# Performance work log

Hardware: AMD Instinct MI355X
Metric: run time of the kernel (lower is better)

The kernel has to match this reference:

```python
import jax, jax.numpy as jnp
import numpy as np

N_NODES = 100000
N_EDGES = 1600000
IN_DIM, HID_DIM, OUT_DIM = 128, 64, 64
NEG_SLOPE = 0.2


def _gat_layer(h_in, src, dst, W, a_src, a_dst, b, n_nodes):
    # h: [N, F_out]
    h = h_in @ W.T
    alpha_src = h @ a_src  # [N]
    alpha_dst = h @ a_dst  # [N]
    # per-edge raw attention logits (edge j->i: src=j, dst=i)
    e = jax.nn.leaky_relu(alpha_src[src] + alpha_dst[dst], NEG_SLOPE)  # [E]
    # segment softmax over incoming edges of each dst node
    m = jax.ops.segment_max(e, dst, num_segments=n_nodes)
    ex = jnp.exp(e - m[dst])
    denom = jax.ops.segment_sum(ex, dst, num_segments=n_nodes)
    alpha = ex / denom[dst]  # [E], denom > 0 thanks to self-loops
    out = jax.ops.segment_sum(h[src] * alpha[:, None], dst, num_segments=n_nodes)
    return out + b


def setup_inputs() -> dict:
    key = jax.random.key(0)
    ks = jax.random.split(key, 12)
    x = jax.random.normal(ks[0], (N_NODES, IN_DIM), dtype=jnp.float32)
    edge_index = jax.random.randint(ks[1], (2, N_EDGES), 0, N_NODES)
    edge_attr = jax.random.normal(ks[2], (N_EDGES, 1), dtype=jnp.float32)
    s1 = 1.0 / np.sqrt(IN_DIM)
    s2 = 1.0 / np.sqrt(HID_DIM)
    W1 = jax.random.normal(ks[3], (HID_DIM, IN_DIM), dtype=jnp.float32) * s1
    att_src1 = jax.random.normal(ks[4], (HID_DIM,), dtype=jnp.float32) * s2
    att_dst1 = jax.random.normal(ks[5], (HID_DIM,), dtype=jnp.float32) * s2
    b1 = jnp.zeros((HID_DIM,), dtype=jnp.float32)
    W2 = jax.random.normal(ks[6], (OUT_DIM, HID_DIM), dtype=jnp.float32) * s2
    att_src2 = jax.random.normal(ks[7], (OUT_DIM,), dtype=jnp.float32) * s2
    att_dst2 = jax.random.normal(ks[8], (OUT_DIM,), dtype=jnp.float32) * s2
    b2 = jnp.zeros((OUT_DIM,), dtype=jnp.float32)
    return {"x": x, "edge_index": edge_index, "edge_attr": edge_attr,
            "W1": W1, "att_src1": att_src1, "att_dst1": att_dst1, "b1": b1,
            "W2": W2, "att_src2": att_src2, "att_dst2": att_dst2, "b2": b2}


def reference(x, edge_index, edge_attr, W1, att_src1, att_dst1, b1,
              W2, att_src2, att_dst2, b2):
    n = x.shape[0]
    # add self-loops (PyG GATConv default); edge_attr unused (edge_dim=None)
    loop = jnp.arange(n, dtype=edge_index.dtype)
    src = jnp.concatenate([edge_index[0], loop])
    dst = jnp.concatenate([edge_index[1], loop])
    h = _gat_layer(x, src, dst, W1, att_src1, att_dst1, b1, n)
    h = jax.nn.relu(h)
    h = _gat_layer(h, src, dst, W2, att_src2, att_dst2, b2, n)
    # global_mean_pool with batch=None -> mean over all nodes, shape [1, F]
    return jnp.mean(h, axis=0, keepdims=True)
```

## Files before the change

kernel.cpp:

```cpp
#include <hip/hip_runtime.h>

#define NEG_SLOPE 0.2f
#define BSHIFT 6
#define NBMAX 2048
#define BCAP 1408
#define CHUNK 8192

__device__ __forceinline__ unsigned short f2b(float x) {
    unsigned u = __float_as_uint(x);
    u += 0x7fff + ((u >> 16) & 1);
    return (unsigned short)(u >> 16);
}
__device__ __forceinline__ float b2f(unsigned short u) {
    return __uint_as_float((unsigned)u << 16);
}

__global__ __launch_bounds__(256) void bin_fixed_kernel(
    const int* __restrict__ ei, int* __restrict__ bcnt,
    int* __restrict__ binned, int E, int NB)
{
    __shared__ int cnt1[NBMAX], rsv[NBMAX], cnt2[NBMAX];
    const int tid = threadIdx.x;
    for (int i = tid; i < NB; i += 256) { cnt1[i] = 0; cnt2[i] = 0; }
    __syncthreads();
    const int start = blockIdx.x * CHUNK;
    const int end = min(start + CHUNK, E);
    for (int i = start + tid; i < end; i += 256)
        atomicAdd(&cnt1[ei[E + i] >> BSHIFT], 1);
    __syncthreads();
    for (int i = tid; i < NB; i += 256)
        rsv[i] = cnt1[i] ? atomicAdd(&bcnt[i], cnt1[i]) : 0;
    __syncthreads();
    for (int i = start + tid; i < end; i += 256) {
        int s = ei[i], d = ei[E + i];
        int b = d >> BSHIFT;
        int r = rsv[b] + atomicAdd(&cnt2[b], 1);
        if (r < BCAP) binned[(size_t)b * BCAP + r] = (s << BSHIFT) | (d & 63);
    }
}

__global__ __launch_bounds__(256) void bscan_kernel(
    const int* __restrict__ bcnt, int* __restrict__ bbase, int NB)
{
    __shared__ int lds[256];
    const int t = threadIdx.x;
    int v[8]; int s = 0;
    #pragma unroll
    for (int j = 0; j < 8; ++j) {
        int i = t * 8 + j;
        v[j] = (i < NB) ? bcnt[i] : 0;
        s += v[j];
    }
    lds[t] = s;
    __syncthreads();
    #pragma unroll
    for (int off = 1; off < 256; off <<= 1) {
        int x = (t >= off) ? lds[t - off] : 0;
        __syncthreads();
        lds[t] += x;
        __syncthreads();
    }
    int excl = (t > 0) ? lds[t - 1] : 0;
    #pragma unroll
    for (int j = 0; j < 8; ++j) {
        int i = t * 8 + j;
        if (i < NB) { bbase[i] = excl + 64 * i; excl += v[j]; }
    }
}

__global__ __launch_bounds__(256) void bucket_csr_kernel(
    const int* __restrict__ binned, const int* __restrict__ bcnt,
    const int* __restrict__ bbase, int* __restrict__ row_ptr,
    int* __restrict__ esrc, int N)
{
    __shared__ int ldeg[64];
    __shared__ int lcur[64];
    const int b = blockIdx.x;
    const int tid = threadIdx.x;
    const int node0 = b << BSHIFT;
    const int cnt = min(bcnt[b], BCAP);
    const int base_e = bbase[b];
    const int* bp = binned + (size_t)b * BCAP;

    if (tid < 64) ldeg[tid] = (node0 + tid < N) ? 1 : 0;
    __syncthreads();
    for (int i = tid; i < cnt; i += 256)
        atomicAdd(&ldeg[bp[i] & 63], 1);
    __syncthreads();
    if (tid < 64) {
        int v = ldeg[tid];
        int inc = v;
        #pragma unroll
        for (int off = 1; off < 64; off <<= 1) {
            int t2 = __shfl_up(inc, off, 64);
            if (tid >= off) inc += t2;
        }
        int excl = inc - v;
        int node = node0 + tid;
        if (node <= N) row_ptr[node] = base_e + excl;
        if (node < N) {
            esrc[base_e + excl] = node;
            lcur[tid] = base_e + excl + 1;
        }
    }
    __syncthreads();
    for (int i = tid; i < cnt; i += 256) {
        int v = bp[i];
        int pos = atomicAdd(&lcur[v & 63], 1);
        esrc[pos] = v >> BSHIFT;
    }
}

template<int K>
__global__ __launch_bounds__(256) void gemm_attn_kernel(
    const float* __restrict__ in, const float* __restrict__ W,
    const float* __restrict__ a_src, const float* __restrict__ a_dst,
    unsigned short* __restrict__ hb, float* __restrict__ asrc,
    float* __restrict__ adst, int N)
{
    constexpr int KB = 64;
    constexpr int NKC = KB / 4;
    constexpr int LDN = 65;
    __shared__ float4 xs4[NKC * LDN];
    __shared__ float4 ws4[NKC * LDN];
    __shared__ float avs[64], avd[64];

    const int tid = threadIdx.x;
    const int node0 = blockIdx.x * 64;
    const int tf = tid & 15;
    const int tn = tid >> 4;

    if (tid < 64) { avs[tid] = a_src[tid]; avd[tid] = a_dst[tid]; }

    float acc[4][4] = {};

    for (int k0 = 0; k0 < K; k0 += KB) {
        if (k0) __syncthreads();
        for (int i = tid; i < 64 * NKC; i += 256) {
            int r = i >> 4, kc = i & 15;
            int node = node0 + r;
            float4 xv = (node < N)
                ? *(const float4*)&in[(size_t)node * K + k0 + 4 * kc]
                : make_float4(0.f, 0.f, 0.f, 0.f);
            xs4[kc * LDN + r] = xv;
            ws4[kc * LDN + r] = *(const float4*)&W[(size_t)r * K + k0 + 4 * kc];
        }
        __syncthreads();

        #pragma unroll 4
        for (int kc = 0; kc < NKC; ++kc) {
            float4 xv[4], wv[4];
            #pragma unroll
            for (int i = 0; i < 4; ++i) xv[i] = xs4[kc * LDN + 4 * tn + i];
            #pragma unroll
            for (int j = 0; j < 4; ++j) wv[j] = ws4[kc * LDN + tf + 16 * j];
            #pragma unroll
            for (int i = 0; i < 4; ++i)
                #pragma unroll
                for (int j = 0; j < 4; ++j) {
                    acc[i][j] = fmaf(xv[i].x, wv[j].x, acc[i][j]);
                    acc[i][j] = fmaf(xv[i].y, wv[j].y, acc[i][j]);
                    acc[i][j] = fmaf(xv[i].z, wv[j].z, acc[i][j]);
                    acc[i][j] = fmaf(xv[i].w, wv[j].w, acc[i][j]);
                }
        }
    }

    #pragma unroll
    for (int i = 0; i < 4; ++i) {
        const int node = node0 + 4 * tn + i;
        const bool valid = node < N;
        float vs = 0.f, vd = 0.f;
        #pragma unroll
        for (int j = 0; j < 4; ++j) {
            int f = tf + 16 * j;
            if (valid) hb[(size_t)node * 64 + f] = f2b(acc[i][j]);
            vs = fmaf(acc[i][j], avs[f], vs);
            vd = fmaf(acc[i][j], avd[f], vd);
        }
        #pragma unroll
        for (int off = 8; off >= 1; off >>= 1) {
            vs += __shfl_down(vs, off, 16);
            vd += __shfl_down(vd, off, 16);
        }
        if (tf == 0 && valid) { asrc[node] = vs; adst[node] = vd; }
    }
}

__global__ __launch_bounds__(256) void aggregate_csr_kernel(
    const int* __restrict__ row_ptr, const int* __restrict__ esrc,
    const float* __restrict__ asrc, const float* __restrict__ adst,
    const unsigned short* __restrict__ hb, const float* __restrict__ bias,
    float* __restrict__ g, int N, int do_relu)
{
    const int node = (int)((blockIdx.x * 256 + threadIdx.x) >> 4);
    const int lane = threadIdx.x & 15;
    if (node >= N) return;
    const int beg = row_ptr[node];
    const int end = row_ptr[node + 1];
    const float ad = adst[node];
    float a0 = 0.f, a1 = 0.f, a2 = 0.f, a3 = 0.f, wsum = 0.f;
    int p = beg;
    for (; p + 4 <= end; p += 4) {
        int s[4]; ushort4 r[4]; float l[4];
        #pragma unroll
        for (int j = 0; j < 4; ++j) s[j] = esrc[p + j];
        #pragma unroll
        for (int j = 0; j < 4; ++j)
            r[j] = *(const ushort4*)(hb + (size_t)s[j] * 64 + lane * 4);
        #pragma unroll
        for (int j = 0; j < 4; ++j) l[j] = asrc[s[j]] + ad;
        #pragma unroll
        for (int j = 0; j < 4; ++j) {
            float ll = (l[j] > 0.f) ? l[j] : NEG_SLOPE * l[j];
            float w = __expf(ll);
            wsum += w;
            a0 = fmaf(w, b2f(r[j].x), a0);
            a1 = fmaf(w, b2f(r[j].y), a1);
            a2 = fmaf(w, b2f(r[j].z), a2);
            a3 = fmaf(w, b2f(r[j].w), a3);
        }
    }
    for (; p < end; ++p) {
        int s = esrc[p];
        ushort4 r = *(const ushort4*)(hb + (size_t)s * 64 + lane * 4);
        float l = asrc[s] + ad;
        l = (l > 0.f) ? l : NEG_SLOPE * l;
        float w = __expf(l);
        wsum += w;
        a0 = fmaf(w, b2f(r.x), a0);
        a1 = fmaf(w, b2f(r.y), a1);
        a2 = fmaf(w, b2f(r.z), a2);
        a3 = fmaf(w, b2f(r.w), a3);
    }
    const float inv = 1.0f / wsum;
    float4 v = make_float4(a0 * inv, a1 * inv, a2 * inv, a3 * inv);
    if (bias) {
        v.x += bias[lane * 4 + 0]; v.y += bias[lane * 4 + 1];
        v.z += bias[lane * 4 + 2]; v.w += bias[lane * 4 + 3];
    }
    if (do_relu) {
        v.x = fmaxf(v.x, 0.f); v.y = fmaxf(v.y, 0.f);
        v.z = fmaxf(v.z, 0.f); v.w = fmaxf(v.w, 0.f);
    }
    *(float4*)&g[(size_t)node * 64 + lane * 4] = v;
}

__global__ __launch_bounds__(256) void pool_kernel(
    const float* __restrict__ g, const float* __restrict__ b2,
    float* __restrict__ out, int N)
{
    __shared__ float red[256];
    const int f = threadIdx.x & 63;
    const int sub = threadIdx.x >> 6;
    float acc = 0.f;
    for (int n = blockIdx.x * 4 + sub; n < N; n += gridDim.x * 4)
        acc += g[(size_t)n * 64 + f];
    red[threadIdx.x] = acc;
    __syncthreads();
    if (threadIdx.x < 64) {
        float s = red[f] + red[64 + f] + red[128 + f] + red[192 + f];
        atomicAdd(out + f, s * (1.0f / (float)N));
        if (blockIdx.x == 0) atomicAdd(out + f, b2[f]);
    }
}

extern "C" void kernel_launch(void* const* d_in, const int* in_sizes, int n_in,
                              void* d_out, int out_size, void* d_ws, size_t ws_size,
                              hipStream_t stream) {
    const float* x   = (const float*)d_in[0];
    const int*   ei  = (const int*)d_in[1];
    const float* W1  = (const float*)d_in[3];
    const float* as1 = (const float*)d_in[4];
    const float* ad1 = (const float*)d_in[5];
    const float* b1  = (const float*)d_in[6];
    const float* W2  = (const float*)d_in[7];
    const float* as2 = (const float*)d_in[8];
    const float* ad2 = (const float*)d_in[9];
    const float* b2  = (const float*)d_in[10];
    float* out = (float*)d_out;

    const int N = in_sizes[0] / 128;
    const int E = in_sizes[1] / 2;
    const int Etot = E + N;
    const int NB = (N + 63) >> BSHIFT;

    auto align4 = [](size_t v) { return (v + 3) & ~(size_t)3; };
    float* ws    = (float*)d_ws;
    size_t off = 0;
    unsigned short* hb = (unsigned short*)(ws + off); off += align4((size_t)N * 32);
    float* g     = ws + off; off += align4((size_t)N * 64);
    float* asrc  = ws + off; off += align4(N);
    float* adst  = ws + off; off += align4(N);
    int* row_ptr = (int*)(ws + off); off += align4(N + 1);
    int* bcnt    = (int*)(ws + off); off += NBMAX;
    int* bbase   = (int*)(ws + off); off += NBMAX;
    int* esrc    = (int*)(ws + off); off += align4(Etot);
    int* binned  = (int*)g;

    const int gemm_blocks  = (N + 63) / 64;
    const int chunk_blocks = (E + CHUNK - 1) / CHUNK;
    const int agg_blocks   = (int)(((size_t)N * 16 + 255) / 256);

    hipMemsetAsync(out, 0, 64 * sizeof(float), stream);
    hipMemsetAsync(bcnt, 0, NB * sizeof(int), stream);

    bin_fixed_kernel<<<chunk_blocks, 256, 0, stream>>>(ei, bcnt, binned, E, NB);
    bscan_kernel<<<1, 256, 0, stream>>>(bcnt, bbase, NB);
    bucket_csr_kernel<<<NB, 256, 0, stream>>>(binned, bcnt, bbase, row_ptr, esrc, N);

    gemm_attn_kernel<128><<<gemm_blocks, 256, 0, stream>>>(x, W1, as1, ad1, hb, asrc, adst, N);
    aggregate_csr_kernel<<<agg_blocks, 256, 0, stream>>>(row_ptr, esrc, asrc, adst, hb, b1, g, N, 1);

    gemm_attn_kernel<64><<<gemm_blocks, 256, 0, stream>>>(g, W2, as2, ad2, hb, asrc, adst, N);
    aggregate_csr_kernel<<<agg_blocks, 256, 0, stream>>>(row_ptr, esrc, asrc, adst, hb, nullptr, g, N, 0);

    pool_kernel<<<512, 256, 0, stream>>>(g, b2, out, N);
}
```

Measured before the change: 311.9 us.

## Replace global atomic bin reservation with per-block histogram and column scan

Splits the fused binning kernel into a per-chunk histogram kernel, a column-wise exclusive scan over blocks, and a scatter kernel that uses the precomputed offsets. This removes the global atomicAdd reservation on bucket counters and makes the bin placement deterministic, and it halves CHUNK to add more blocks. In exchange it reads the edge list twice and adds two extra launches plus a histogram buffer (NBLK×NB ints) to write and read back. The column scan is a serial loop over about 390 blocks per bucket. bscan now clamps the bucket totals to BCAP.

```diff
diff --git a/kernel.cpp b/kernel.cpp
--- a/kernel.cpp
+++ b/kernel.cpp
@@ -4,7 +4,7 @@
 #define BSHIFT 6
 #define NBMAX 2048
 #define BCAP 1408
-#define CHUNK 8192
+#define CHUNK 4096
 
 __device__ __forceinline__ unsigned short f2b(float x) {
     unsigned u = __float_as_uint(x);
@@ -15,32 +15,70 @@
     return __uint_as_float((unsigned)u << 16);
 }
 
-__global__ __launch_bounds__(256) void bin_fixed_kernel(
-    const int* __restrict__ ei, int* __restrict__ bcnt,
-    int* __restrict__ binned, int E, int NB)
-{
-    __shared__ int cnt1[NBMAX], rsv[NBMAX], cnt2[NBMAX];
+__global__ __launch_bounds__(256) void hist_kernel(
+    const int* __restrict__ ei, int* __restrict__ hist, int E, int NB)
+{
+    __shared__ int cnt[NBMAX];
     const int tid = threadIdx.x;
-    for (int i = tid; i < NB; i += 256) { cnt1[i] = 0; cnt2[i] = 0; }
+    for (int i = tid; i < NB; i += 256) cnt[i] = 0;
     __syncthreads();
     const int start = blockIdx.x * CHUNK;
     const int end = min(start + CHUNK, E);
     for (int i = start + tid; i < end; i += 256)
-        atomicAdd(&cnt1[ei[E + i] >> BSHIFT], 1);
+        atomicAdd(&cnt[ei[E + i] >> BSHIFT], 1);
     __syncthreads();
     for (int i = tid; i < NB; i += 256)
-        rsv[i] = cnt1[i] ? atomicAdd(&bcnt[i], cnt1[i]) : 0;
-    __syncthreads();
+        hist[(size_t)blockIdx.x * NB + i] = cnt[i];
+}
+
+__global__ __launch_bounds__(256) void colscan_kernel(
+    int* __restrict__ hist, int* __restrict__ btotal, int NB, int NBLK)
+{
+    const int b = blockIdx.x * 256 + threadIdx.x;
+    if (b >= NB) return;
+    int run = 0;
+    int blk = 0;
+    for (; blk + 8 <= NBLK; blk += 8) {
+        int w[8];
+        #pragma unroll
+        for (int j = 0; j < 8; ++j) w[j] = hist[(size_t)(blk + j) * NB + b];
+        #pragma unroll
+        for (int j = 0; j < 8; ++j) {
+            hist[(size_t)(blk + j) * NB + b] = run;
+            run += w[j];
+        }
+    }
+    for (; blk < NBLK; ++blk) {
+        int w = hist[(size_t)blk * NB + b];
+        hist[(size_t)blk * NB + b] = run;
+        run += w;
+    }
+    btotal[b] = run;
+}
+
+__global__ __launch_bounds__(256) void scatter_kernel(
+    const int* __restrict__ ei, const int* __restrict__ hist,
+    int* __restrict__ binned, int E, int NB)
+{
+    __shared__ int base[NBMAX], cnt2[NBMAX];
+    const int tid = threadIdx.x;
+    for (int i = tid; i < NB; i += 256) {
+        base[i] = hist[(size_t)blockIdx.x * NB + i];
+        cnt2[i] = 0;
+    }
+    __syncthreads();
+    const int start = blockIdx.x * CHUNK;
+    const int end = min(start + CHUNK, E);
     for (int i = start + tid; i < end; i += 256) {
         int s = ei[i], d = ei[E + i];
         int b = d >> BSHIFT;
-        int r = rsv[b] + atomicAdd(&cnt2[b], 1);
+        int r = base[b] + atomicAdd(&cnt2[b], 1);
         if (r < BCAP) binned[(size_t)b * BCAP + r] = (s << BSHIFT) | (d & 63);
     }
 }
 
 __global__ __launch_bounds__(256) void bscan_kernel(
-    const int* __restrict__ bcnt, int* __restrict__ bbase, int NB)
+    const int* __restrict__ btotal, int* __restrict__ bbase, int NB)
 {
     __shared__ int lds[256];
     const int t = threadIdx.x;
@@ -48,7 +86,7 @@
     #pragma unroll
     for (int j = 0; j < 8; ++j) {
         int i = t * 8 + j;
-        v[j] = (i < NB) ? bcnt[i] : 0;
+        v[j] = (i < NB) ? min(btotal[i], BCAP) : 0;
         s += v[j];
     }
     lds[t] = s;
@@ -69,7 +107,7 @@
 }
 
 __global__ __launch_bounds__(256) void bucket_csr_kernel(
-    const int* __restrict__ binned, const int* __restrict__ bcnt,
+    const int* __restrict__ binned, const int* __restrict__ btotal,
     const int* __restrict__ bbase, int* __restrict__ row_ptr,
     int* __restrict__ esrc, int N)
 {
@@ -78,7 +116,7 @@
     const int b = blockIdx.x;
     const int tid = threadIdx.x;
     const int node0 = b << BSHIFT;
-    const int cnt = min(bcnt[b], BCAP);
+    const int cnt = min(btotal[b], BCAP);
     const int base_e = bbase[b];
     const int* bp = binned + (size_t)b * BCAP;
 
@@ -284,6 +322,7 @@
     const int E = in_sizes[1] / 2;
     const int Etot = E + N;
     const int NB = (N + 63) >> BSHIFT;
+    const int NBLK = (E + CHUNK - 1) / CHUNK;
 
     auto align4 = [](size_t v) { return (v + 3) & ~(size_t)3; };
     float* ws    = (float*)d_ws;
@@ -293,21 +332,22 @@
     float* asrc  = ws + off; off += align4(N);
     float* adst  = ws + off; off += align4(N);
     int* row_ptr = (int*)(ws + off); off += align4(N + 1);
-    int* bcnt    = (int*)(ws + off); off += NBMAX;
+    int* btotal  = (int*)(ws + off); off += NBMAX;
     int* bbase   = (int*)(ws + off); off += NBMAX;
+    int* hist    = (int*)(ws + off); off += align4((size_t)NBLK * NB);
     int* esrc    = (int*)(ws + off); off += align4(Etot);
     int* binned  = (int*)g;
 
-    const int gemm_blocks  = (N + 63) / 64;
-    const int chunk_blocks = (E + CHUNK - 1) / CHUNK;
-    const int agg_blocks   = (int)(((size_t)N * 16 + 255) / 256);
+    const int gemm_blocks = (N + 63) / 64;
+    const int agg_blocks  = (int)(((size_t)N * 16 + 255) / 256);
 
     hipMemsetAsync(out, 0, 64 * sizeof(float), stream);
-    hipMemsetAsync(bcnt, 0, NB * sizeof(int), stream);
-
-    bin_fixed_kernel<<<chunk_blocks, 256, 0, stream>>>(ei, bcnt, binned, E, NB);
-    bscan_kernel<<<1, 256, 0, stream>>>(bcnt, bbase, NB);
-    bucket_csr_kernel<<<NB, 256, 0, stream>>>(binned, bcnt, bbase, row_ptr, esrc, N);
+
+    hist_kernel<<<NBLK, 256, 0, stream>>>(ei, hist, E, NB);
+    colscan_kernel<<<(NB + 255) / 256, 256, 0, stream>>>(hist, btotal, NB, NBLK);
+    scatter_kernel<<<NBLK, 256, 0, stream>>>(ei, hist, binned, E, NB);
+    bscan_kernel<<<1, 256, 0, stream>>>(btotal, bbase, NB);
+    bucket_csr_kernel<<<NB, 256, 0, stream>>>(binned, btotal, bbase, row_ptr, esrc, N);
 
     gemm_attn_kernel<128><<<gemm_blocks, 256, 0, stream>>>(x, W1, as1, ad1, hb, asrc, adst, N);
     aggregate_csr_kernel<<<agg_blocks, 256, 0, stream>>>(row_ptr, esrc, asrc, adst, hb, b1, g, N, 1);
```

After: 319.0 us. 1.02x slower.
